# Performance work log

Measured on AMD Instinct MI355X. Metric: run time of the kernel, lower is better.

## Reference

```python
import jax, jax.numpy as jnp
import numpy as np

B, S, D, H, E = 32, 128, 128, 128, 64
NUM_SLOTS = 10
K = NUM_SLOTS + 1
TIME_WINDOW = 3600.0
DIST_WINDOW = 1.0
VOCAB = 10000
OUT = 10000
PRE_LEN = 16


def _xavier(k, shape):
    fan_in, fan_out = shape[-2], shape[-1]
    std = (2.0 / (fan_in + fan_out)) ** 0.5
    return jax.random.normal(k, shape, jnp.float32) * std


def setup_inputs() -> dict:
    key = jax.random.key(0)
    ks = jax.random.split(key, 12)
    full_seq = jax.random.randint(ks[0], (B, S), 0, VOCAB)
    valid_len = jnp.full((B,), S, dtype=jnp.int32)  # no padding: history + pre fill whole seq
    dt = jax.random.uniform(ks[1], (B, S), jnp.float32) * 600.0  # inter-event gaps [0,600)s
    timestamp = jnp.cumsum(dt, axis=1)  # monotonically increasing timestamps
    lat = jax.random.uniform(ks[2], (B, S), jnp.float32)
    lng = jax.random.uniform(ks[3], (B, S), jnp.float32)
    embed_table = _xavier(ks[4], (VOCAB, D))
    time_weights = _xavier(ks[5], (K, D, E))
    dist_weights = _xavier(ks[6], (K, E, H))
    hidden_weights = _xavier(ks[7], (H, H))
    W1 = _xavier(ks[8], (H, 4 * H))
    b1 = jnp.zeros((4 * H,), jnp.float32)
    W2 = _xavier(ks[9], (4 * H, OUT))
    b2 = jnp.zeros((OUT,), jnp.float32)
    return dict(full_seq=full_seq, valid_len=valid_len, pre_len=PRE_LEN,
                timestamp=timestamp, lat=lat, lng=lng, embed_table=embed_table,
                time_weights=time_weights, dist_weights=dist_weights,
                hidden_weights=hidden_weights, W1=W1, b1=b1, W2=W2, b2=b2)


def reference(full_seq, valid_len, pre_len, timestamp, lat, lng, embed_table,
              time_weights, dist_weights, hidden_weights, W1, b1, W2, b2):
    # valid_len == S for all samples, so the per-sample restack in the torch code
    # (history || prediction || zero-pad) is the identity: sequential_input == cat_input.
    x = embed_table[full_seq]                      # (B,S,D) encoder input (cols :-3)
    ts = timestamp
    latlng = jnp.stack([lat, lng], axis=-1)        # (B,S,2)

    # time_delta[b,i,j] = ts[b,i] - ts[b,j]
    td = ts[:, :, None] - ts[:, None, :]           # (B,S,S)
    seq_ar = jnp.arange(S)
    valid = (valid_len[:, None] > seq_ar[None, :])[:, None, :]  # (B,1,S) mask over j
    context_mask = (td <= TIME_WINDOW) & (td >= 0.0) & valid    # (B,S,S)
    # growing-context window: step i sees only j <= i
    causal = seq_ar[None, :] <= seq_ar[:, None]    # (S,S), True where j<=i
    m = context_mask & causal[None, :, :]

    dist = jnp.sqrt(((latlng[:, :, None, :] - latlng[:, None, :, :]) ** 2).sum(-1))  # (B,S,S)
    tc = jnp.floor(jnp.clip(td, 0.0, TIME_WINDOW) / TIME_WINDOW * NUM_SLOTS).astype(jnp.int32)
    dc = jnp.floor(jnp.clip(dist, 0.0, DIST_WINDOW) / DIST_WINDOW * NUM_SLOTS).astype(jnp.int32)

    # Associatively reordered STRNN cell: instead of gathering per-(i,j) weight
    # matrices and forming (x @ Wt) @ Wd per pair, contract x with every time slot
    # once, then select slots via one-hot and reduce over slots for the dist side.
    dtype = x.dtype
    v_slots = jnp.einsum('bji,kie->bjke', x, time_weights)        # (B,S,K,E)
    oh_t = jax.nn.one_hot(tc, K, dtype=dtype) * m[..., None].astype(dtype)  # (B,S,S,K)
    v = jnp.einsum('bjke,bijk->bije', v_slots, oh_t)              # (B,S,S,E) masked x@Wt
    oh_d = jax.nn.one_hot(dc, K, dtype=dtype)                     # (B,S,S,K)
    agg = jnp.einsum('bije,bijk->bike', v, oh_d)                  # (B,S,K,E)
    x_cand = jnp.einsum('bike,keh->bih', agg, dist_weights)       # (B,S,H)

    # hidden-state recurrence: h_i = sigmoid(x_cand_i + h_{i-1} @ Wh)
    def step(h, xc):
        h_new = jax.nn.sigmoid(xc + h @ hidden_weights)
        return h_new, h_new
    h0 = jnp.zeros((B, H), dtype)
    _, outs = jax.lax.scan(step, h0, jnp.swapaxes(x_cand, 0, 1))  # (S,B,H)
    rnn_out = jnp.swapaxes(outs, 0, 1)                            # (B,S,H)

    # valid_len == S: rnn_out[i, s-pre_len-1 : s-1] is a static slice
    rnn_out_pre = rnn_out[:, S - pre_len - 1: S - 1]              # (B,pre_len,H)
    # out_linear: Dropout(0.1) is identity at inference
    out = jnp.tanh(rnn_out_pre @ W1 + b1) @ W2 + b2               # (B,pre_len,OUT)
    return out
```

## Files before the change

kernel.cpp:

```cpp
#include <hip/hip_runtime.h>
#include <hip/hip_bf16.h>
#include <math.h>

#define BB 32
#define SS 128
#define DD 128
#define HH 128
#define EE 64
#define KK_SLOTS 11
#define NKE 704
#define PRE 16
#define OUTN 10000
#define H4 512
#define VOCAB 10000

#define WARMUP 20
#define NSTEP (WARMUP + 1)
#define R0 91
#define NRNN 36

typedef unsigned short u16;
typedef __attribute__((ext_vector_type(8))) short bf16x8;
typedef __attribute__((ext_vector_type(4))) float f32x4;

__device__ __forceinline__ u16 f2bf(float f) {
    unsigned u = __float_as_uint(f);
    u = u + 0x7fffu + ((u >> 16) & 1u);
    return (u16)(u >> 16);
}
__device__ __forceinline__ float bf2f(u16 h) {
    return __uint_as_float(((unsigned)h) << 16);
}

__device__ __forceinline__ void load_lds16(const void* g, void* l) {
    __builtin_amdgcn_global_load_lds(
        (const __attribute__((address_space(1))) unsigned int*)g,
        (__attribute__((address_space(3))) unsigned int*)l,
        16, 0, 0);
}

#define PREP_GC_BLKS   512
#define PREP_W2_BLKS   (313 * 16)
#define PREP_TW_BLKS   (KK_SLOTS * 8)
#define PREP_DW_BLKS   (22 * 4)
#define PREP_W1B_BLKS  64

__device__ __forceinline__ void tr32(const float* __restrict__ src,
                                     u16* __restrict__ dst, int R, int C,
                                     int r0, int c0, float (*tile)[33]) {
    const int tx = threadIdx.x & 31, ty = threadIdx.x >> 5;
    #pragma unroll
    for (int i = 0; i < 32; i += 8) {
        const int r = r0 + ty + i, c = c0 + tx;
        tile[ty + i][tx] = (r < R && c < C) ? src[(size_t)r * C + c] : 0.f;
    }
    __syncthreads();
    #pragma unroll
    for (int i = 0; i < 32; i += 8) {
        const int c = c0 + ty + i, r = r0 + tx;
        if (c < C && r < R) dst[(size_t)c * R + r] = f2bf(tile[tx][ty + i]);
    }
}

__global__ __launch_bounds__(256) void prep_kernel(
    const float* __restrict__ embed, const int* __restrict__ full_seq,
    const float* __restrict__ tw, const float* __restrict__ dw,
    const float* __restrict__ W1, const float* __restrict__ W2,
    u16* __restrict__ acmp, u16* __restrict__ twT, u16* __restrict__ dwT,
    u16* __restrict__ w1b, u16* __restrict__ w2T)
{
    __shared__ float tile[32][33];
    int blk = blockIdx.x;

    if (blk < PREP_GC_BLKS) {
        const int g = blk * 1024 + threadIdx.x * 4;
        const int m = g >> 7, c = g & 127;
        const int arow = full_seq[m];
        const float4 v = *(const float4*)(embed + (size_t)arow * DD + c);
        ushort4 o;
        o.x = f2bf(v.x); o.y = f2bf(v.y); o.z = f2bf(v.z); o.w = f2bf(v.w);
        *(ushort4*)(acmp + g) = o;
        return;
    }
    blk -= PREP_GC_BLKS;
    if (blk < PREP_W2_BLKS) {
        tr32(W2, w2T, H4, OUTN, (blk / 313) * 32, (blk % 313) * 32, tile);
        return;
    }
    blk -= PREP_W2_BLKS;
    if (blk < PREP_TW_BLKS) {
        const int bo = blk / 8, t = blk % 8;
        tr32(tw + (size_t)bo * DD * EE, twT + (size_t)bo * DD * EE,
             DD, EE, (t / 2) * 32, (t % 2) * 32, tile);
        return;
    }
    blk -= PREP_TW_BLKS;
    if (blk < PREP_DW_BLKS) {
        tr32(dw, dwT, NKE, HH, (blk / 4) * 32, (blk % 4) * 32, tile);
        return;
    }
    blk -= PREP_DW_BLKS;
    {
        const int g = blk * 1024 + threadIdx.x * 4;
        const float4 v = *(const float4*)(W1 + g);
        ushort4 o;
        o.x = f2bf(v.x); o.y = f2bf(v.y); o.z = f2bf(v.z); o.w = f2bf(v.w);
        *(ushort4*)(w1b + g) = o;
    }
}

template<int BM, int SK>
__global__ __launch_bounds__(256) void gemm_mfma(
    const u16* __restrict__ A, const u16* __restrict__ BT,
    void* __restrict__ Cout, const float* __restrict__ bias,
    int M, int N, int Kd, int act, int outbf)
{
    __shared__ u16 As[BM * 32];
    __shared__ u16 Bs[128 * 32];

    const int tid  = threadIdx.x;
    const int lane = tid & 63;
    const int wid  = tid >> 6;
    const int quad = lane >> 4;
    const int l16  = lane & 15;
    const int m0 = blockIdx.y * BM;
    const int n0 = blockIdx.x * 128;

    constexpr int WM = (BM == 128) ? 64 : 32;
    constexpr int NI = WM / 16;
    const int wm = (wid >> 1) * WM;
    const int wn = (wid & 1) * 64;

    const int ksteps = Kd / 32;
    int kz0 = 0, kz1 = ksteps;
    if (SK > 1) {
        const int per = (ksteps + SK - 1) / SK;
        kz0 = blockIdx.z * per;
        kz1 = kz0 + per; if (kz1 > ksteps) kz1 = ksteps;
    }

    const int rA0 = tid >> 2;
    const int kc  = (tid & 3) * 16;

    const long arow0 = m0 + rA0;
    const long arow1 = m0 + 64 + rA0;
    int nrow0 = n0 + rA0;      if (nrow0 > N - 1) nrow0 = N - 1;
    int nrow1 = n0 + 64 + rA0; if (nrow1 > N - 1) nrow1 = N - 1;

    const size_t Kb = (size_t)Kd * 2;
    const char* Ab = (const char*)A;
    const char* Bb = (const char*)BT;
    char* AsB = (char*)As;
    char* BsB = (char*)Bs;

    f32x4 acc[NI][4] = {};

    for (int ks = kz0; ks < kz1; ++ks) {
        const size_t k0 = (size_t)ks * 64;
        __syncthreads();
        load_lds16(Ab + arow0 * Kb + k0 + kc, AsB + wid * 1024);
        if constexpr (BM == 128)
            load_lds16(Ab + arow1 * Kb + k0 + kc, AsB + 4096 + wid * 1024);
        load_lds16(Bb + (size_t)nrow0 * Kb + k0 + kc, BsB + wid * 1024);
        load_lds16(Bb + (size_t)nrow1 * Kb + k0 + kc, BsB + 4096 + wid * 1024);
        __syncthreads();

        bf16x8 af[NI], bfr[4];
        #pragma unroll
        for (int t = 0; t < NI; ++t)
            af[t] = *(const bf16x8*)&As[(wm + t * 16 + l16) * 32 + quad * 8];
        #pragma unroll
        for (int t = 0; t < 4; ++t)
            bfr[t] = *(const bf16x8*)&Bs[(wn + t * 16 + l16) * 32 + quad * 8];

        #pragma unroll
        for (int i = 0; i < NI; ++i)
            #pragma unroll
            for (int j = 0; j < 4; ++j)
                acc[i][j] = __builtin_amdgcn_mfma_f32_16x16x32_bf16(
                    af[i], bfr[j], acc[i][j], 0, 0, 0);
    }

    float* outF = (float*)Cout;
    if (SK > 1) outF += (size_t)blockIdx.z * M * N;
    #pragma unroll
    for (int i = 0; i < NI; ++i) {
        #pragma unroll
        for (int j = 0; j < 4; ++j) {
            const int col = n0 + wn + j * 16 + l16;
            if (col >= N) continue;
            const float bv = bias ? bias[col] : 0.f;
            #pragma unroll
            for (int r = 0; r < 4; ++r) {
                const int row = m0 + wm + i * 16 + quad * 4 + r;
                float v = acc[i][j][r] + bv;
                if (act == 1) v = tanhf(v);
                if (outbf) ((u16*)Cout)[(size_t)row * N + col] = f2bf(v);
                else       outF[(size_t)row * N + col] = v;
            }
        }
    }
}

__global__ __launch_bounds__(64) void agg_kernel(
    const u16* __restrict__ vslots, const float* __restrict__ ts,
    const float* __restrict__ lat, const float* __restrict__ lng,
    const int* __restrict__ valid_len, u16* __restrict__ agg)
{
    __shared__ unsigned char tcdc[SS];
    const int blk = blockIdx.x;
    const int e = threadIdx.x;
    const int b = blk / NRNN;
    const int i = R0 + (blk % NRNN);

    const float tsi  = ts[b * SS + i];
    const float lati = lat[b * SS + i];
    const float lngi = lng[b * SS + i];
    const int vlen = valid_len[b];
    const int jmax = (i < vlen - 1) ? i : (vlen - 1);

    unsigned long long mask[2];
    #pragma unroll
    for (int half = 0; half < 2; ++half) {
        const int j = half * 64 + e;
        const float td = tsi - ts[b * SS + j];
        const bool ok = (j <= jmax) & (td >= 0.f) & (td <= 3600.f);
        const int tc = (int)floorf(fminf(fmaxf(td, 0.f), 3600.f) / 3600.f * 10.f);
        const float dx = lati - lat[b * SS + j];
        const float dy = lngi - lng[b * SS + j];
        const float dist = sqrtf(dx * dx + dy * dy);
        const int dc = (int)floorf(fminf(fmaxf(dist, 0.f), 1.f) * 10.f);
        tcdc[j] = (unsigned char)((tc << 4) | dc);
        mask[half] = __ballot(ok);
    }
    __syncthreads();

    float accs[KK_SLOTS];
    #pragma unroll
    for (int s = 0; s < KK_SLOTS; ++s) accs[s] = 0.f;

    const u16* vb = vslots + (size_t)b * SS * NKE;
    #pragma unroll
    for (int half = 0; half < 2; ++half) {
        unsigned long long m = mask[half];
        while (m) {
            const int j = __ffsll((long long)m) - 1 + half * 64;
            m &= m - 1;
            const int code = tcdc[j & 127];
            const int tc = code >> 4, dc = code & 15;
            const float v = bf2f(vb[(size_t)(j) * NKE + tc * 64 + e]);
            #pragma unroll
            for (int s = 0; s < KK_SLOTS; ++s)
                accs[s] += (dc == s) ? v : 0.f;
        }
    }

    u16* out = agg + (size_t)blk * NKE;
    #pragma unroll
    for (int s = 0; s < KK_SLOTS; ++s) out[s * 64 + e] = f2bf(accs[s]);
}

__global__ __launch_bounds__(256, 1) void rnn_mlp_kernel(
    const float* __restrict__ xcand, const float* __restrict__ Wh,
    const u16* __restrict__ w1b, const float* __restrict__ b1,
    u16* __restrict__ t1)
{
    __shared__ float xcs[NSTEP * HH];
    __shared__ float hbuf[2][HH];
    __shared__ float part[256];
    const int blk = blockIdx.x;
    const int b  = blk >> 4;
    const int oi = blk & 15;
    const int tid = threadIdx.x;
    const int t    = tid & 127;
    const int half = tid >> 7;

    float w[64];
    #pragma unroll
    for (int dd = 0; dd < 64; ++dd)
        w[dd] = Wh[(half * 64 + dd) * HH + t];

    const float* xc0 = xcand + (size_t)b * NRNN * HH;
    const float* xc1 = xc0 + (size_t)BB * NRNN * HH;
    for (int idx = tid; idx < NSTEP * HH; idx += 256) {
        const int s = idx >> 7, c = idx & 127;
        xcs[idx] = xc0[(oi + s) * HH + c] + xc1[(oi + s) * HH + c];
    }

    if (tid < HH) hbuf[0][tid] = 0.f;
    __syncthreads();

    int cur = 0;
    for (int s = 0; s < NSTEP; ++s) {
        const float* hb = &hbuf[cur][half * 64];
        float a0 = 0.f, a1 = 0.f, a2 = 0.f, a3 = 0.f;
        float a4 = 0.f, a5 = 0.f, a6 = 0.f, a7 = 0.f;
        #pragma unroll
        for (int dd = 0; dd < 64; dd += 8) {
            const float4 h0 = *(const float4*)&hb[dd];
            const float4 h1 = *(const float4*)&hb[dd + 4];
            a0 += h0.x * w[dd + 0]; a1 += h0.y * w[dd + 1];
            a2 += h0.z * w[dd + 2]; a3 += h0.w * w[dd + 3];
            a4 += h1.x * w[dd + 4]; a5 += h1.y * w[dd + 5];
            a6 += h1.z * w[dd + 6]; a7 += h1.w * w[dd + 7];
        }
        part[tid] = ((a0 + a1) + (a2 + a3)) + ((a4 + a5) + (a6 + a7));
        __syncthreads();
        if (tid < HH) {
            const float sum = xcs[s * HH + tid] + part[tid] + part[tid + 128];
            hbuf[cur ^ 1][tid] = 1.f / (1.f + __expf(-sum));
        }
        __syncthreads();
        cur ^= 1;
    }

    const int c0 = tid * 2;
    float o0 = b1[c0], o1 = b1[c0 + 1];
    #pragma unroll 8
    for (int d = 0; d < HH; ++d) {
        const float hd = hbuf[cur][d];
        const ushort2 wv = *(const ushort2*)(w1b + (size_t)d * H4 + c0);
        o0 += hd * bf2f(wv.x); o1 += hd * bf2f(wv.y);
    }
    ushort2 ov;
    ov.x = f2bf(tanhf(o0)); ov.y = f2bf(tanhf(o1));
    *(ushort2*)(t1 + ((size_t)b * PRE + oi) * H4 + c0) = ov;
}

extern "C" void kernel_launch(void* const* d_in, const int* in_sizes, int n_in,
                              void* d_out, int out_size, void* d_ws, size_t ws_size,
                              hipStream_t stream)
{
    const int*   full_seq  = (const int*)d_in[0];
    const int*   valid_len = (const int*)d_in[1];
    const float* timestamp = (const float*)d_in[3];
    const float* lat       = (const float*)d_in[4];
    const float* lng       = (const float*)d_in[5];
    const float* embed     = (const float*)d_in[6];
    const float* tw        = (const float*)d_in[7];
    const float* dw        = (const float*)d_in[8];
    const float* Wh        = (const float*)d_in[9];
    const float* W1        = (const float*)d_in[10];
    const float* b1        = (const float*)d_in[11];
    const float* W2        = (const float*)d_in[12];
    const float* b2        = (const float*)d_in[13];
    float* out = (float*)d_out;

    const int MR = BB * NRNN;
    const int M1 = BB * SS;

    char* p = (char*)d_ws;
    u16*   acmp   = (u16*)p;   p += (size_t)M1 * DD * 2;
    u16*   vslots = (u16*)p;   p += (size_t)M1 * NKE * 2;
    u16*   aggb   = (u16*)p;   p += (size_t)MR * NKE * 2;
    float* xcand  = (float*)p; p += (size_t)2 * MR * HH * 4;
    u16*   t1     = (u16*)p;   p += (size_t)BB * PRE * H4 * 2;
    u16*   twT    = (u16*)p;   p += (size_t)KK_SLOTS * EE * DD * 2;
    u16*   dwT    = (u16*)p;   p += (size_t)NKE * HH * 2;
    u16*   w1b    = (u16*)p;   p += (size_t)HH * H4 * 2;
    u16*   w2T    = (u16*)p;   p += (size_t)OUTN * H4 * 2;

    const int prep_blocks = PREP_GC_BLKS + PREP_W2_BLKS + PREP_TW_BLKS +
                            PREP_DW_BLKS + PREP_W1B_BLKS;

    prep_kernel<<<dim3(prep_blocks), 256, 0, stream>>>(
        embed, full_seq, tw, dw, W1, W2, acmp, twT, dwT, w1b, w2T);

    gemm_mfma<128, 1><<<dim3((NKE + 127) / 128, M1 / 128), 256, 0, stream>>>(
        acmp, twT, vslots, nullptr, M1, NKE, DD, 0, 1);

    agg_kernel<<<dim3(MR), 64, 0, stream>>>(
        vslots, timestamp, lat, lng, valid_len, aggb);

    gemm_mfma<64, 2><<<dim3(1, MR / 64, 2), 256, 0, stream>>>(
        aggb, dwT, xcand, nullptr, MR, HH, NKE, 0, 0);

    rnn_mlp_kernel<<<dim3(BB * PRE), 256, 0, stream>>>(
        xcand, Wh, w1b, b1, t1);

    gemm_mfma<64, 1><<<dim3((OUTN + 127) / 128, (BB * PRE) / 64), 256, 0, stream>>>(
        t1, w2T, out, b2, BB * PRE, OUTN, H4, 0, 0);
}
```

Baseline: 176.3 us.

## Fuse dist-weight projection into aggregation kernel and drop split-K GEMM

The aggregation kernel now keeps its per-row aggregated slot vector in shared memory and directly computes the x_cand row with scalar FMAs against a bf16 copy of dist_weights, removing the separate split-K MFMA GEMM launch, the bf16 agg round trip and the split-K partial sum. dist_weights is converted in place rather than transposed. The final output GEMM switches from 64-row to 128-row tiles, halving its block count. The fused projection uses scalar FP32 math per 64-thread block instead of matrix cores, trading one kernel launch and some memory traffic for more ALU work per block.

```diff
diff --git a/kernel.cpp b/kernel.cpp
--- a/kernel.cpp
+++ b/kernel.cpp
@@ -42,7 +42,7 @@
 #define PREP_GC_BLKS   512
 #define PREP_W2_BLKS   (313 * 16)
 #define PREP_TW_BLKS   (KK_SLOTS * 8)
-#define PREP_DW_BLKS   (22 * 4)
+#define PREP_DW_BLKS   88
 #define PREP_W1B_BLKS  64
 
 __device__ __forceinline__ void tr32(const float* __restrict__ src,
@@ -62,11 +62,19 @@
     }
 }
 
+__device__ __forceinline__ void conv4(const float* __restrict__ src,
+                                      u16* __restrict__ dst, int g) {
+    const float4 v = *(const float4*)(src + g);
+    ushort4 o;
+    o.x = f2bf(v.x); o.y = f2bf(v.y); o.z = f2bf(v.z); o.w = f2bf(v.w);
+    *(ushort4*)(dst + g) = o;
+}
+
 __global__ __launch_bounds__(256) void prep_kernel(
     const float* __restrict__ embed, const int* __restrict__ full_seq,
     const float* __restrict__ tw, const float* __restrict__ dw,
     const float* __restrict__ W1, const float* __restrict__ W2,
-    u16* __restrict__ acmp, u16* __restrict__ twT, u16* __restrict__ dwT,
+    u16* __restrict__ acmp, u16* __restrict__ twT, u16* __restrict__ dwb,
     u16* __restrict__ w1b, u16* __restrict__ w2T)
 {
     __shared__ float tile[32][33];
@@ -96,20 +104,16 @@
     }
     blk -= PREP_TW_BLKS;
     if (blk < PREP_DW_BLKS) {
-        tr32(dw, dwT, NKE, HH, (blk / 4) * 32, (blk % 4) * 32, tile);
+        conv4(dw, dwb, blk * 1024 + threadIdx.x * 4);
         return;
     }
     blk -= PREP_DW_BLKS;
     {
-        const int g = blk * 1024 + threadIdx.x * 4;
-        const float4 v = *(const float4*)(W1 + g);
-        ushort4 o;
-        o.x = f2bf(v.x); o.y = f2bf(v.y); o.z = f2bf(v.z); o.w = f2bf(v.w);
-        *(ushort4*)(w1b + g) = o;
-    }
-}
-
-template<int BM, int SK>
+        conv4(W1, w1b, blk * 1024 + threadIdx.x * 4);
+    }
+}
+
+template<int BM>
 __global__ __launch_bounds__(256) void gemm_mfma(
     const u16* __restrict__ A, const u16* __restrict__ BT,
     void* __restrict__ Cout, const float* __restrict__ bias,
@@ -132,12 +136,6 @@
     const int wn = (wid & 1) * 64;
 
     const int ksteps = Kd / 32;
-    int kz0 = 0, kz1 = ksteps;
-    if (SK > 1) {
-        const int per = (ksteps + SK - 1) / SK;
-        kz0 = blockIdx.z * per;
-        kz1 = kz0 + per; if (kz1 > ksteps) kz1 = ksteps;
-    }
 
     const int rA0 = tid >> 2;
     const int kc  = (tid & 3) * 16;
@@ -155,7 +153,7 @@
 
     f32x4 acc[NI][4] = {};
 
-    for (int ks = kz0; ks < kz1; ++ks) {
+    for (int ks = 0; ks < ksteps; ++ks) {
         const size_t k0 = (size_t)ks * 64;
         __syncthreads();
         load_lds16(Ab + arow0 * Kb + k0 + kc, AsB + wid * 1024);
@@ -182,7 +180,6 @@
     }
 
     float* outF = (float*)Cout;
-    if (SK > 1) outF += (size_t)blockIdx.z * M * N;
     #pragma unroll
     for (int i = 0; i < NI; ++i) {
         #pragma unroll
@@ -202,12 +199,14 @@
     }
 }
 
-__global__ __launch_bounds__(64) void agg_kernel(
+__global__ __launch_bounds__(64) void agg_xc_kernel(
     const u16* __restrict__ vslots, const float* __restrict__ ts,
     const float* __restrict__ lat, const float* __restrict__ lng,
-    const int* __restrict__ valid_len, u16* __restrict__ agg)
+    const int* __restrict__ valid_len, const u16* __restrict__ dwb,
+    float* __restrict__ xcand)
 {
     __shared__ unsigned char tcdc[SS];
+    __shared__ float aggsh[NKE];
     const int blk = blockIdx.x;
     const int e = threadIdx.x;
     const int b = blk / NRNN;
@@ -255,9 +254,21 @@
         }
     }
 
-    u16* out = agg + (size_t)blk * NKE;
-    #pragma unroll
-    for (int s = 0; s < KK_SLOTS; ++s) out[s * 64 + e] = f2bf(accs[s]);
+    #pragma unroll
+    for (int s = 0; s < KK_SLOTS; ++s) aggsh[s * 64 + e] = accs[s];
+    __syncthreads();
+
+    const int c0 = e * 2;
+    float o0 = 0.f, o1 = 0.f;
+    #pragma unroll 4
+    for (int k = 0; k < NKE; ++k) {
+        const float a = aggsh[k];
+        const ushort2 wv = *(const ushort2*)(dwb + (size_t)k * HH + c0);
+        o0 += a * bf2f(wv.x);
+        o1 += a * bf2f(wv.y);
+    }
+    float2 ov; ov.x = o0; ov.y = o1;
+    *(float2*)(xcand + (size_t)blk * HH + c0) = ov;
 }
 
 __global__ __launch_bounds__(256, 1) void rnn_mlp_kernel(
@@ -281,10 +292,9 @@
         w[dd] = Wh[(half * 64 + dd) * HH + t];
 
     const float* xc0 = xcand + (size_t)b * NRNN * HH;
-    const float* xc1 = xc0 + (size_t)BB * NRNN * HH;
     for (int idx = tid; idx < NSTEP * HH; idx += 256) {
         const int s = idx >> 7, c = idx & 127;
-        xcs[idx] = xc0[(oi + s) * HH + c] + xc1[(oi + s) * HH + c];
+        xcs[idx] = xc0[(oi + s) * HH + c];
     }
 
     if (tid < HH) hbuf[0][tid] = 0.f;
@@ -352,11 +362,10 @@
     char* p = (char*)d_ws;
     u16*   acmp   = (u16*)p;   p += (size_t)M1 * DD * 2;
     u16*   vslots = (u16*)p;   p += (size_t)M1 * NKE * 2;
-    u16*   aggb   = (u16*)p;   p += (size_t)MR * NKE * 2;
-    float* xcand  = (float*)p; p += (size_t)2 * MR * HH * 4;
+    float* xcand  = (float*)p; p += (size_t)MR * HH * 4;
     u16*   t1     = (u16*)p;   p += (size_t)BB * PRE * H4 * 2;
     u16*   twT    = (u16*)p;   p += (size_t)KK_SLOTS * EE * DD * 2;
-    u16*   dwT    = (u16*)p;   p += (size_t)NKE * HH * 2;
+    u16*   dwb    = (u16*)p;   p += (size_t)NKE * HH * 2;
     u16*   w1b    = (u16*)p;   p += (size_t)HH * H4 * 2;
     u16*   w2T    = (u16*)p;   p += (size_t)OUTN * H4 * 2;
 
@@ -364,20 +373,17 @@
                             PREP_DW_BLKS + PREP_W1B_BLKS;
 
     prep_kernel<<<dim3(prep_blocks), 256, 0, stream>>>(
-        embed, full_seq, tw, dw, W1, W2, acmp, twT, dwT, w1b, w2T);
-
-    gemm_mfma<128, 1><<<dim3((NKE + 127) / 128, M1 / 128), 256, 0, stream>>>(
+        embed, full_seq, tw, dw, W1, W2, acmp, twT, dwb, w1b, w2T);
+
+    gemm_mfma<128><<<dim3((NKE + 127) / 128, M1 / 128), 256, 0, stream>>>(
         acmp, twT, vslots, nullptr, M1, NKE, DD, 0, 1);
 
-    agg_kernel<<<dim3(MR), 64, 0, stream>>>(
-        vslots, timestamp, lat, lng, valid_len, aggb);
-
-    gemm_mfma<64, 2><<<dim3(1, MR / 64, 2), 256, 0, stream>>>(
-        aggb, dwT, xcand, nullptr, MR, HH, NKE, 0, 0);
+    agg_xc_kernel<<<dim3(MR), 64, 0, stream>>>(
+        vslots, timestamp, lat, lng, valid_len, dwb, xcand);
 
     rnn_mlp_kernel<<<dim3(BB * PRE), 256, 0, stream>>>(
         xcand, Wh, w1b, b1, t1);
 
-    gemm_mfma<64, 1><<<dim3((OUTN + 127) / 128, (BB * PRE) / 64), 256, 0, stream>>>(
+    gemm_mfma<128><<<dim3((OUTN + 127) / 128, (BB * PRE) / 128), 256, 0, stream>>>(
         t1, w2T, out, b2, BB * PRE, OUTN, H4, 0, 0);
 }
```

After: 210.1 us. +19.2%, slower.
